# Kernel optimization log

Measured on AMD Instinct MI355X. Metric: run time of the kernel, lower is better.

Reference implementation:

```python
import jax, jax.numpy as jnp
import numpy as np

N_NODES = 50000
EMBED = 64
N_EDGES = 1250000
N_USERS = 25000
BATCH, K = 1024, 100


def setup_inputs() -> dict:
    key = jax.random.key(0)
    ks = jax.random.split(key, 8)
    stdv = 1.0 / np.sqrt(EMBED)
    emb = jax.random.uniform(ks[0], (N_NODES, EMBED), jnp.float32, -stdv, stdv)
    # nn.Linear default init: U(-1/sqrt(fan_in), 1/sqrt(fan_in))
    lim = 1.0 / np.sqrt(EMBED)
    W0 = jax.random.uniform(ks[1], (EMBED, EMBED), jnp.float32, -lim, lim)
    b0 = jax.random.uniform(ks[2], (EMBED,), jnp.float32, -lim, lim)
    W1 = jax.random.uniform(ks[3], (EMBED, EMBED), jnp.float32, -lim, lim)
    b1 = jax.random.uniform(ks[4], (EMBED,), jnp.float32, -lim, lim)
    src = jax.random.randint(ks[5], (N_EDGES,), 0, N_NODES, jnp.int32)
    dst = jax.random.randint(ks[6], (N_EDGES,), 0, N_NODES, jnp.int32)
    user_index = jax.random.randint(ks[7], (BATCH, K), 0, N_USERS, jnp.int32)
    item_index = jax.random.randint(jax.random.fold_in(key, 99), (BATCH, K), 0, N_NODES, jnp.int32)
    return {"embeddings": emb, "W0": W0, "b0": b0, "W1": W1, "b1": b1,
            "src": src, "dst": dst, "user_index": user_index, "item_index": item_index}


def _mean_aggregate(h, src, dst):
    # copy_src gather + mailbox mean: mean of src features over incoming edges per dst
    msg_sum = jax.ops.segment_sum(h[src], dst, num_segments=N_NODES)  # [N, D]
    deg = jax.ops.segment_sum(jnp.ones((src.shape[0],), h.dtype), dst, num_segments=N_NODES)
    return msg_sum / jnp.maximum(deg, 1.0)[:, None]


def reference(embeddings, W0, b0, W1, b1, src, dst, user_index, item_index):
    h = embeddings
    for W, b in ((W0, b0), (W1, b1)):
        agg = _mean_aggregate(h, src, dst)          # [N, D] mean mailbox
        h = jnp.tanh(agg @ W.T + b)                  # NodeUpdate: Linear + Tanh
    user = h[user_index]                             # [B, K, D]
    item = h[item_index]                             # [B, K, D]
    score = jnp.sum(user * item, axis=2)             # [B, K]
    return score
```

## Files before the change

kernel.cpp:

```cpp
#include <hip/hip_runtime.h>

#define N_NODES 50000
#define N_EDGES 1250000
#define EMBED 64
#define N_PAIRS (1024 * 100)
#define BSHIFT 7
#define BSIZE 128
#define NBUCK 391
#define CB 153
#define FAST_MAX 3584
#define CAP 4096
#define GEMV_BLKS ((N_NODES + 63) / 64)

__device__ inline float bf2f(unsigned short u) {
    return __uint_as_float(((unsigned)u) << 16);
}
__device__ inline unsigned short f2bf(float x) {
    unsigned u = __float_as_uint(x);
    u += 0x7FFF + ((u >> 16) & 1);
    return (unsigned short)(u >> 16);
}

__global__ __launch_bounds__(1024) void hist_kernel(const int* __restrict__ dst,
                                                    int* __restrict__ counts,
                                                    int* __restrict__ btot) {
    __shared__ int hl[NBUCK];
    int t = threadIdx.x, b = blockIdx.x;
    for (int i = t; i < NBUCK; i += 1024) hl[i] = 0;
    __syncthreads();
    #pragma unroll
    for (int rep = 0; rep < 2; ++rep) {
        int i4 = b * 2048 + rep * 1024 + t;
        if (i4 < N_EDGES / 4) {
            int4 d = ((const int4*)dst)[i4];
            atomicAdd(&hl[d.x >> BSHIFT], 1);
            atomicAdd(&hl[d.y >> BSHIFT], 1);
            atomicAdd(&hl[d.z >> BSHIFT], 1);
            atomicAdd(&hl[d.w >> BSHIFT], 1);
        }
    }
    __syncthreads();
    for (int i = t; i < NBUCK; i += 1024) {
        int v = hl[i];
        counts[i * CB + b] = v;
        if (v) atomicAdd(&btot[i], v);
    }
}

__global__ __launch_bounds__(512) void bscan_kernel(const int* __restrict__ btot,
                                                    int* __restrict__ base) {
    __shared__ int ws[8];
    int t = threadIdx.x, lane = t & 63, wid = t >> 6;
    int v = (t < NBUCK) ? btot[t] : 0;
    int incl = v;
    #pragma unroll
    for (int off = 1; off < 64; off <<= 1) {
        int o = __shfl_up(incl, off);
        if (lane >= off) incl += o;
    }
    if (lane == 63) ws[wid] = incl;
    __syncthreads();
    if (t < 8) {
        int x = ws[t];
        #pragma unroll
        for (int off = 1; off < 8; off <<= 1) {
            int o = __shfl_up(x, off);
            if (t >= off) x += o;
        }
        ws[t] = x;
    }
    __syncthreads();
    int ex = ((wid > 0) ? ws[wid - 1] : 0) + incl - v;
    if (t < NBUCK) base[t] = ex;
    if (t == 0) base[NBUCK] = N_EDGES;
}

__global__ __launch_bounds__(64) void offs_kernel(const int* __restrict__ counts,
                                                  const int* __restrict__ base,
                                                  int* __restrict__ offs) {
    int k = blockIdx.x, lane = threadIdx.x;
    const int* rowp = counts + (size_t)k * CB;
    int* orow = offs + (size_t)k * CB;
    int carry = base[k];
    #pragma unroll
    for (int tile = 0; tile < 3; ++tile) {
        int b = tile * 64 + lane;
        int v = (b < CB) ? rowp[b] : 0;
        int incl = v;
        #pragma unroll
        for (int off = 1; off < 64; off <<= 1) {
            int o = __shfl_up(incl, off);
            if (lane >= off) incl += o;
        }
        if (b < CB) orow[b] = carry + incl - v;
        carry += __shfl(incl, 63);
    }
}

__global__ __launch_bounds__(1024) void scatter_kernel(const int* __restrict__ src,
                                                       const int* __restrict__ dst,
                                                       const int* __restrict__ offs,
                                                       unsigned int* __restrict__ pairs) {
    __shared__ int cur[NBUCK];
    int t = threadIdx.x, b = blockIdx.x;
    for (int i = t; i < NBUCK; i += 1024) cur[i] = offs[i * CB + b];
    __syncthreads();
    #pragma unroll
    for (int rep = 0; rep < 2; ++rep) {
        int i4 = b * 2048 + rep * 1024 + t;
        if (i4 < N_EDGES / 4) {
            int4 s4 = ((const int4*)src)[i4];
            int4 d4 = ((const int4*)dst)[i4];
            int p;
            p = atomicAdd(&cur[d4.x >> BSHIFT], 1);
            pairs[p] = ((unsigned)(d4.x & (BSIZE - 1)) << 16) | (unsigned)s4.x;
            p = atomicAdd(&cur[d4.y >> BSHIFT], 1);
            pairs[p] = ((unsigned)(d4.y & (BSIZE - 1)) << 16) | (unsigned)s4.y;
            p = atomicAdd(&cur[d4.z >> BSHIFT], 1);
            pairs[p] = ((unsigned)(d4.z & (BSIZE - 1)) << 16) | (unsigned)s4.z;
            p = atomicAdd(&cur[d4.w >> BSHIFT], 1);
            pairs[p] = ((unsigned)(d4.w & (BSIZE - 1)) << 16) | (unsigned)s4.w;
        }
    }
}

#define SMEM_BYTES 34832
__global__ __launch_bounds__(256) void sortgemv_kernel(const unsigned int* __restrict__ pairs,
                                                       const int* __restrict__ base,
                                                       int* __restrict__ rowp,
                                                       int* __restrict__ degv,
                                                       int* __restrict__ col,
                                                       const float* __restrict__ emb,
                                                       const float* __restrict__ W,
                                                       unsigned short* __restrict__ g) {
    __shared__ __align__(16) char smem[SMEM_BYTES];
    int t = threadIdx.x;
    if (blockIdx.x < NBUCK) {
        unsigned* ebuf = (unsigned*)smem;
        int* staged    = (int*)(smem + 16384);
        int* hist      = (int*)(smem + 32768);
        int* cur       = (int*)(smem + 33280);
        int* wtot      = (int*)(smem + 33792);
        int* ptotS     = (int*)(smem + 33796);
        int k = blockIdx.x;
        int lane = t & 63, wid = t >> 6;
        int nstart = k * BSIZE;
        int nodes = min(BSIZE, N_NODES - nstart);
        int estart = base[k], eend = base[k + 1];
        int cnt = eend - estart;
        int cbase = k << 12;
        if (t < BSIZE) hist[t] = 0;
        __syncthreads();
        if (cnt <= FAST_MAX) {
            for (int i = t; i < cnt; i += 256) {
                unsigned w = pairs[estart + i];
                ebuf[i] = w;
                atomicAdd(&hist[w >> 16], 1);
            }
            __syncthreads();
            if (t < BSIZE) {
                int dgv = hist[t];
                int pd = (dgv + 3) & ~3;
                int incl = pd;
                #pragma unroll
                for (int off = 1; off < 64; off <<= 1) {
                    int o = __shfl_up(incl, off);
                    if (lane >= off) incl += o;
                }
                if (t == 63) *wtot = incl;
                __syncthreads();
                int ex = incl - pd + ((wid == 1) ? *wtot : 0);
                cur[t] = ex;
                if (t == BSIZE - 1) *ptotS = ex + pd;
                if (t < nodes) {
                    rowp[nstart + t] = cbase + ex;
                    degv[nstart + t] = dgv;
                }
            } else {
                __syncthreads();
            }
            __syncthreads();
            int ptot = *ptotS;
            for (int i = t; i < ptot; i += 256) staged[i] = N_NODES;
            __syncthreads();
            for (int i = t; i < cnt; i += 256) {
                unsigned w = ebuf[i];
                int pos = atomicAdd(&cur[w >> 16], 1);
                staged[pos] = (int)(w & 0xFFFFu);
            }
            __syncthreads();
            for (int i = t; i < ptot; i += 256) col[cbase + i] = staged[i];
        } else {
            for (int i = t; i < cnt; i += 256)
                atomicAdd(&hist[pairs[estart + i] >> 16], 1);
            __syncthreads();
            if (t < BSIZE) {
                int dgv = hist[t];
                int pd = (dgv + 3) & ~3;
                int incl = pd;
                #pragma unroll
                for (int off = 1; off < 64; off <<= 1) {
                    int o = __shfl_up(incl, off);
                    if (lane >= off) incl += o;
                }
                if (t == 63) *wtot = incl;
                __syncthreads();
                int ex = incl - pd + ((wid == 1) ? *wtot : 0);
                cur[t] = ex;
                if (t == BSIZE - 1) *ptotS = ex + pd;
                if (t < nodes) {
                    rowp[nstart + t] = cbase + ex;
                    degv[nstart + t] = dgv;
                }
            } else {
                __syncthreads();
            }
            __syncthreads();
            int ptot = *ptotS;
            for (int i = t; i < ptot; i += 256) col[cbase + i] = N_NODES;
            __syncthreads();
            for (int i = t; i < cnt; i += 256) {
                unsigned w = pairs[estart + i];
                int pos = atomicAdd(&cur[w >> 16], 1);
                col[cbase + pos] = (int)(w & 0xFFFFu);
            }
        }
    } else {
        float (*hL)[64] = (float (*)[64])smem;
        float (*Wl)[65] = (float (*)[65])(smem + 16384);
        int gb = blockIdx.x - NBUCK;
        int nstart = gb * 64;
        int lane = t & 63, wid = t >> 6;
        for (int i = t; i < 4096; i += 256) Wl[i & 63][i >> 6] = W[i];
        int nrem = min(64, N_NODES - nstart);
        for (int i = t; i < nrem * 16; i += 256)
            ((float4*)hL)[i] = ((const float4*)(emb + (size_t)nstart * EMBED))[i];
        if (gb == GEMV_BLKS - 1 && t < 64) g[(size_t)N_NODES * EMBED + t] = 0;
        __syncthreads();
        for (int n = wid; n < nrem; n += 4) {
            float x = 0.f;
            #pragma unroll
            for (int d = 0; d < 64; ++d)
                x += hL[n][d] * Wl[d][lane];
            g[(size_t)(nstart + n) * EMBED + lane] = f2bf(x);
        }
    }
}

__global__ __launch_bounds__(256) void gemv_kernel(const float* __restrict__ h,
                                                   const float* __restrict__ W,
                                                   unsigned short* __restrict__ g) {
    __shared__ float hL[64][64];
    __shared__ float Wl[64][65];
    int t = threadIdx.x;
    int nstart = blockIdx.x * 64;
    int lane = t & 63, wid = t >> 6;
    for (int i = t; i < 4096; i += 256) Wl[i & 63][i >> 6] = W[i];
    int nrem = min(64, N_NODES - nstart);
    for (int i = t; i < nrem * 16; i += 256)
        ((float4*)hL)[i] = ((const float4*)(h + (size_t)nstart * EMBED))[i];
    __syncthreads();
    for (int n = wid; n < nrem; n += 4) {
        float x = 0.f;
        #pragma unroll
        for (int d = 0; d < 64; ++d)
            x += hL[n][d] * Wl[d][lane];
        g[(size_t)(nstart + n) * EMBED + lane] = f2bf(x);
    }
}

__global__ __launch_bounds__(256) void agg_kernel(const unsigned short* __restrict__ g,
                                                  const float* __restrict__ bias,
                                                  const int* __restrict__ rowp,
                                                  const int* __restrict__ degv,
                                                  const int* __restrict__ col,
                                                  float* __restrict__ hout) {
    int t = threadIdx.x;
    int wid = t >> 6, lane = t & 63;
    int node = blockIdx.x * 4 + wid;
    int gg = lane >> 4, d16 = lane & 15;
    int start = rowp[node];
    int dg = degv[node];
    int pcnt = (dg + 3) & ~3;
    int endp = start + pcnt;
    float4 bb = ((const float4*)bias)[d16];
    float4 acc = {0.f, 0.f, 0.f, 0.f};
    int e = start;
    for (; e + 16 <= endp; e += 16) {
        int s0 = col[e + gg];
        int s1 = col[e + 4 + gg];
        int s2 = col[e + 8 + gg];
        int s3 = col[e + 12 + gg];
        ushort4 v0 = ((const ushort4*)(g + (size_t)s0 * EMBED))[d16];
        ushort4 v1 = ((const ushort4*)(g + (size_t)s1 * EMBED))[d16];
        ushort4 v2 = ((const ushort4*)(g + (size_t)s2 * EMBED))[d16];
        ushort4 v3 = ((const ushort4*)(g + (size_t)s3 * EMBED))[d16];
        acc.x += (bf2f(v0.x) + bf2f(v1.x)) + (bf2f(v2.x) + bf2f(v3.x));
        acc.y += (bf2f(v0.y) + bf2f(v1.y)) + (bf2f(v2.y) + bf2f(v3.y));
        acc.z += (bf2f(v0.z) + bf2f(v1.z)) + (bf2f(v2.z) + bf2f(v3.z));
        acc.w += (bf2f(v0.w) + bf2f(v1.w)) + (bf2f(v2.w) + bf2f(v3.w));
    }
    for (; e < endp; e += 4) {
        int s0 = col[e + gg];
        ushort4 v0 = ((const ushort4*)(g + (size_t)s0 * EMBED))[d16];
        acc.x += bf2f(v0.x);
        acc.y += bf2f(v0.y);
        acc.z += bf2f(v0.z);
        acc.w += bf2f(v0.w);
    }
    #pragma unroll
    for (int off = 16; off < 64; off <<= 1) {
        acc.x += __shfl_xor(acc.x, off);
        acc.y += __shfl_xor(acc.y, off);
        acc.z += __shfl_xor(acc.z, off);
        acc.w += __shfl_xor(acc.w, off);
    }
    float inv = (dg > 0) ? 1.0f / (float)dg : 0.f;
    if (gg == 0) {
        float4 o;
        o.x = tanhf(acc.x * inv + bb.x);
        o.y = tanhf(acc.y * inv + bb.y);
        o.z = tanhf(acc.z * inv + bb.z);
        o.w = tanhf(acc.w * inv + bb.w);
        ((float4*)(hout + (size_t)node * EMBED))[d16] = o;
    }
}

__global__ __launch_bounds__(256) void score_kernel(const float* __restrict__ h,
                                                    const int* __restrict__ ui,
                                                    const int* __restrict__ ii,
                                                    float* __restrict__ out) {
    int t = threadIdx.x;
    int idx = blockIdx.x * 16 + (t >> 4);
    int d16 = t & 15;
    int u = ui[idx];
    int v = ii[idx];
    float4 a = ((const float4*)(h + (size_t)u * EMBED))[d16];
    float4 b = ((const float4*)(h + (size_t)v * EMBED))[d16];
    float p = a.x * b.x + a.y * b.y + a.z * b.z + a.w * b.w;
    #pragma unroll
    for (int off = 8; off > 0; off >>= 1)
        p += __shfl_xor(p, off);
    if (d16 == 0) out[idx] = p;
}

extern "C" void kernel_launch(void* const* d_in, const int* in_sizes, int n_in,
                              void* d_out, int out_size, void* d_ws, size_t ws_size,
                              hipStream_t stream) {
    const float* emb = (const float*)d_in[0];
    const float* W0  = (const float*)d_in[1];
    const float* b0  = (const float*)d_in[2];
    const float* W1  = (const float*)d_in[3];
    const float* b1  = (const float*)d_in[4];
    const int* src   = (const int*)d_in[5];
    const int* dst   = (const int*)d_in[6];
    const int* ui    = (const int*)d_in[7];
    const int* ii    = (const int*)d_in[8];
    float* out = (float*)d_out;

    char* p = (char*)d_ws;
    auto alloc = [&](size_t bytes) {
        char* r = p;
        p += (bytes + 255) & ~(size_t)255;
        return r;
    };
    int* counts          = (int*)alloc(sizeof(int) * NBUCK * CB);
    int* offs            = (int*)alloc(sizeof(int) * NBUCK * CB);
    int* btot            = (int*)alloc(sizeof(int) * NBUCK);
    int* base            = (int*)alloc(sizeof(int) * (NBUCK + 1));
    int* rowp            = (int*)alloc(sizeof(int) * N_NODES);
    int* degv            = (int*)alloc(sizeof(int) * N_NODES);
    unsigned* pairs      = (unsigned*)alloc(sizeof(unsigned) * N_EDGES);
    int* col             = (int*)alloc(sizeof(int) * NBUCK * CAP);
    unsigned short* gbuf = (unsigned short*)alloc(sizeof(unsigned short) * (N_NODES + 1) * EMBED);
    float* hbuf          = (float*)alloc(sizeof(float) * N_NODES * EMBED);

    hipMemsetAsync(btot, 0, sizeof(int) * NBUCK, stream);
    hist_kernel<<<CB, 1024, 0, stream>>>(dst, counts, btot);
    bscan_kernel<<<1, 512, 0, stream>>>(btot, base);
    offs_kernel<<<NBUCK, 64, 0, stream>>>(counts, base, offs);
    scatter_kernel<<<CB, 1024, 0, stream>>>(src, dst, offs, pairs);
    sortgemv_kernel<<<NBUCK + GEMV_BLKS, 256, 0, stream>>>(pairs, base, rowp, degv, col,
                                                           emb, W0, gbuf);
    agg_kernel<<<N_NODES / 4, 256, 0, stream>>>(gbuf, b0, rowp, degv, col, hbuf);
    gemv_kernel<<<GEMV_BLKS, 256, 0, stream>>>(hbuf, W1, gbuf);
    agg_kernel<<<N_NODES / 4, 256, 0, stream>>>(gbuf, b1, rowp, degv, col, hbuf);
    score_kernel<<<N_PAIRS / 16, 256, 0, stream>>>(hbuf, ui, ii, out);
}
```

Baseline: 220.7 us.

## Fuse layer-one aggregation with layer-two GEMV and store final embeddings as bf16

Merges the first mean-aggregation and the second-layer 64x64 projection into one kernel. Each wave writes its node's tanh output row to shared memory and multiplies it by W1 held in LDS, so the fp32 intermediate h no longer makes a round trip through global memory and one launch is removed. The final layer output is now stored as bf16, which halves the bytes the score kernel gathers. The cost is that every 4-node block reloads the full 16KB W1 into LDS, and the final embeddings lose precision.

```diff
diff --git a/kernel.cpp b/kernel.cpp
--- a/kernel.cpp
+++ b/kernel.cpp
@@ -247,34 +247,78 @@
     }
 }
 
-__global__ __launch_bounds__(256) void gemv_kernel(const float* __restrict__ h,
-                                                   const float* __restrict__ W,
-                                                   unsigned short* __restrict__ g) {
-    __shared__ float hL[64][64];
+__global__ __launch_bounds__(256) void agg_gemv_kernel(const unsigned short* __restrict__ g,
+                                                       const float* __restrict__ bias,
+                                                       const float* __restrict__ W,
+                                                       const int* __restrict__ rowp,
+                                                       const int* __restrict__ degv,
+                                                       const int* __restrict__ col,
+                                                       unsigned short* __restrict__ g2) {
     __shared__ float Wl[64][65];
+    __shared__ float rowL[4][64];
     int t = threadIdx.x;
-    int nstart = blockIdx.x * 64;
-    int lane = t & 63, wid = t >> 6;
+    int wid = t >> 6, lane = t & 63;
     for (int i = t; i < 4096; i += 256) Wl[i & 63][i >> 6] = W[i];
-    int nrem = min(64, N_NODES - nstart);
-    for (int i = t; i < nrem * 16; i += 256)
-        ((float4*)hL)[i] = ((const float4*)(h + (size_t)nstart * EMBED))[i];
-    __syncthreads();
-    for (int n = wid; n < nrem; n += 4) {
-        float x = 0.f;
-        #pragma unroll
-        for (int d = 0; d < 64; ++d)
-            x += hL[n][d] * Wl[d][lane];
-        g[(size_t)(nstart + n) * EMBED + lane] = f2bf(x);
-    }
-}
-
-__global__ __launch_bounds__(256) void agg_kernel(const unsigned short* __restrict__ g,
-                                                  const float* __restrict__ bias,
-                                                  const int* __restrict__ rowp,
-                                                  const int* __restrict__ degv,
-                                                  const int* __restrict__ col,
-                                                  float* __restrict__ hout) {
+    int node = blockIdx.x * 4 + wid;
+    if (blockIdx.x == 0 && t < 64) g2[(size_t)N_NODES * EMBED + t] = 0;
+    int gg = lane >> 4, d16 = lane & 15;
+    int start = rowp[node];
+    int dg = degv[node];
+    int pcnt = (dg + 3) & ~3;
+    int endp = start + pcnt;
+    float4 bb = ((const float4*)bias)[d16];
+    float4 acc = {0.f, 0.f, 0.f, 0.f};
+    int e = start;
+    for (; e + 16 <= endp; e += 16) {
+        int s0 = col[e + gg];
+        int s1 = col[e + 4 + gg];
+        int s2 = col[e + 8 + gg];
+        int s3 = col[e + 12 + gg];
+        ushort4 v0 = ((const ushort4*)(g + (size_t)s0 * EMBED))[d16];
+        ushort4 v1 = ((const ushort4*)(g + (size_t)s1 * EMBED))[d16];
+        ushort4 v2 = ((const ushort4*)(g + (size_t)s2 * EMBED))[d16];
+        ushort4 v3 = ((const ushort4*)(g + (size_t)s3 * EMBED))[d16];
+        acc.x += (bf2f(v0.x) + bf2f(v1.x)) + (bf2f(v2.x) + bf2f(v3.x));
+        acc.y += (bf2f(v0.y) + bf2f(v1.y)) + (bf2f(v2.y) + bf2f(v3.y));
+        acc.z += (bf2f(v0.z) + bf2f(v1.z)) + (bf2f(v2.z) + bf2f(v3.z));
+        acc.w += (bf2f(v0.w) + bf2f(v1.w)) + (bf2f(v2.w) + bf2f(v3.w));
+    }
+    for (; e < endp; e += 4) {
+        int s0 = col[e + gg];
+        ushort4 v0 = ((const ushort4*)(g + (size_t)s0 * EMBED))[d16];
+        acc.x += bf2f(v0.x);
+        acc.y += bf2f(v0.y);
+        acc.z += bf2f(v0.z);
+        acc.w += bf2f(v0.w);
+    }
+    #pragma unroll
+    for (int off = 16; off < 64; off <<= 1) {
+        acc.x += __shfl_xor(acc.x, off);
+        acc.y += __shfl_xor(acc.y, off);
+        acc.z += __shfl_xor(acc.z, off);
+        acc.w += __shfl_xor(acc.w, off);
+    }
+    float inv = (dg > 0) ? 1.0f / (float)dg : 0.f;
+    if (gg == 0) {
+        rowL[wid][d16 * 4 + 0] = tanhf(acc.x * inv + bb.x);
+        rowL[wid][d16 * 4 + 1] = tanhf(acc.y * inv + bb.y);
+        rowL[wid][d16 * 4 + 2] = tanhf(acc.z * inv + bb.z);
+        rowL[wid][d16 * 4 + 3] = tanhf(acc.w * inv + bb.w);
+    }
+    __syncthreads();
+    float x = 0.f;
+    #pragma unroll
+    for (int d = 0; d < 64; ++d)
+        x += rowL[wid][d] * Wl[d][lane];
+    g2[(size_t)node * EMBED + lane] = f2bf(x);
+}
+
+__global__ __launch_bounds__(256) void agg_out_kernel(const unsigned short* __restrict__ g,
+                                                      const float* __restrict__ bias,
+                                                      const int* __restrict__ rowp,
+                                                      const int* __restrict__ degv,
+                                                      const int* __restrict__ col,
+                                                      unsigned short* __restrict__ hout) {
     int t = threadIdx.x;
     int wid = t >> 6, lane = t & 63;
     int node = blockIdx.x * 4 + wid;
@@ -317,16 +361,16 @@
     }
     float inv = (dg > 0) ? 1.0f / (float)dg : 0.f;
     if (gg == 0) {
-        float4 o;
-        o.x = tanhf(acc.x * inv + bb.x);
-        o.y = tanhf(acc.y * inv + bb.y);
-        o.z = tanhf(acc.z * inv + bb.z);
-        o.w = tanhf(acc.w * inv + bb.w);
-        ((float4*)(hout + (size_t)node * EMBED))[d16] = o;
-    }
-}
-
-__global__ __launch_bounds__(256) void score_kernel(const float* __restrict__ h,
+        ushort4 o;
+        o.x = f2bf(tanhf(acc.x * inv + bb.x));
+        o.y = f2bf(tanhf(acc.y * inv + bb.y));
+        o.z = f2bf(tanhf(acc.z * inv + bb.z));
+        o.w = f2bf(tanhf(acc.w * inv + bb.w));
+        ((ushort4*)(hout + (size_t)node * EMBED))[d16] = o;
+    }
+}
+
+__global__ __launch_bounds__(256) void score_kernel(const unsigned short* __restrict__ h,
                                                     const int* __restrict__ ui,
                                                     const int* __restrict__ ii,
                                                     float* __restrict__ out) {
@@ -335,9 +379,10 @@
     int d16 = t & 15;
     int u = ui[idx];
     int v = ii[idx];
-    float4 a = ((const float4*)(h + (size_t)u * EMBED))[d16];
-    float4 b = ((const float4*)(h + (size_t)v * EMBED))[d16];
-    float p = a.x * b.x + a.y * b.y + a.z * b.z + a.w * b.w;
+    ushort4 a4 = ((const ushort4*)(h + (size_t)u * EMBED))[d16];
+    ushort4 b4 = ((const ushort4*)(h + (size_t)v * EMBED))[d16];
+    float p = bf2f(a4.x) * bf2f(b4.x) + bf2f(a4.y) * bf2f(b4.y) +
+              bf2f(a4.z) * bf2f(b4.z) + bf2f(a4.w) * bf2f(b4.w);
     #pragma unroll
     for (int off = 8; off > 0; off >>= 1)
         p += __shfl_xor(p, off);
@@ -364,16 +409,17 @@
         p += (bytes + 255) & ~(size_t)255;
         return r;
     };
-    int* counts          = (int*)alloc(sizeof(int) * NBUCK * CB);
-    int* offs            = (int*)alloc(sizeof(int) * NBUCK * CB);
-    int* btot            = (int*)alloc(sizeof(int) * NBUCK);
-    int* base            = (int*)alloc(sizeof(int) * (NBUCK + 1));
-    int* rowp            = (int*)alloc(sizeof(int) * N_NODES);
-    int* degv            = (int*)alloc(sizeof(int) * N_NODES);
-    unsigned* pairs      = (unsigned*)alloc(sizeof(unsigned) * N_EDGES);
-    int* col             = (int*)alloc(sizeof(int) * NBUCK * CAP);
-    unsigned short* gbuf = (unsigned short*)alloc(sizeof(unsigned short) * (N_NODES + 1) * EMBED);
-    float* hbuf          = (float*)alloc(sizeof(float) * N_NODES * EMBED);
+    int* counts           = (int*)alloc(sizeof(int) * NBUCK * CB);
+    int* offs             = (int*)alloc(sizeof(int) * NBUCK * CB);
+    int* btot             = (int*)alloc(sizeof(int) * NBUCK);
+    int* base             = (int*)alloc(sizeof(int) * (NBUCK + 1));
+    int* rowp             = (int*)alloc(sizeof(int) * N_NODES);
+    int* degv             = (int*)alloc(sizeof(int) * N_NODES);
+    unsigned* pairs       = (unsigned*)alloc(sizeof(unsigned) * N_EDGES);
+    int* col              = (int*)alloc(sizeof(int) * NBUCK * CAP);
+    unsigned short* g1buf = (unsigned short*)alloc(sizeof(unsigned short) * (N_NODES + 1) * EMBED);
+    unsigned short* g2buf = (unsigned short*)alloc(sizeof(unsigned short) * (N_NODES + 1) * EMBED);
+    unsigned short* hbuf  = (unsigned short*)alloc(sizeof(unsigned short) * N_NODES * EMBED);
 
     hipMemsetAsync(btot, 0, sizeof(int) * NBUCK, stream);
     hist_kernel<<<CB, 1024, 0, stream>>>(dst, counts, btot);
@@ -381,9 +427,8 @@
     offs_kernel<<<NBUCK, 64, 0, stream>>>(counts, base, offs);
     scatter_kernel<<<CB, 1024, 0, stream>>>(src, dst, offs, pairs);
     sortgemv_kernel<<<NBUCK + GEMV_BLKS, 256, 0, stream>>>(pairs, base, rowp, degv, col,
-                                                           emb, W0, gbuf);
-    agg_kernel<<<N_NODES / 4, 256, 0, stream>>>(gbuf, b0, rowp, degv, col, hbuf);
-    gemv_kernel<<<GEMV_BLKS, 256, 0, stream>>>(hbuf, W1, gbuf);
-    agg_kernel<<<N_NODES / 4, 256, 0, stream>>>(gbuf, b1, rowp, degv, col, hbuf);
+                                                           emb, W0, g1buf);
+    agg_gemv_kernel<<<N_NODES / 4, 256, 0, stream>>>(g1buf, b0, W1, rowp, degv, col, g2buf);
+    agg_out_kernel<<<N_NODES / 4, 256, 0, stream>>>(g2buf, b1, rowp, degv, col, hbuf);
     score_kernel<<<N_PAIRS / 16, 256, 0, stream>>>(hbuf, ui, ii, out);
 }
```

New measurement: 210.1 us. 4.8% less time.
